# Kernel tuning notes

Hardware: AMD Instinct MI355X
Metric: run time of the kernel (lower is better)

## Reference

```python
import jax, jax.numpy as jnp
import numpy as np

NUM_ITEMS = 50000
IN_FEATS = 64
H_FEATS = 64
NUM_EDGES = 800000


def setup_inputs() -> dict:
    key = jax.random.key(0)
    ks = jax.random.split(key, 12)
    s_in = 1.0 / np.sqrt(IN_FEATS)
    s_h = 1.0 / np.sqrt(H_FEATS)
    return {
        "embed": jax.random.normal(ks[0], (NUM_ITEMS, IN_FEATS), jnp.float32),
        "W1_self": jax.random.normal(ks[1], (IN_FEATS, H_FEATS), jnp.float32) * s_in,
        "W1_neigh": jax.random.normal(ks[2], (IN_FEATS, H_FEATS), jnp.float32) * s_in,
        "b1": jax.random.normal(ks[3], (H_FEATS,), jnp.float32) * s_in,
        "W2_self": jax.random.normal(ks[4], (H_FEATS, H_FEATS), jnp.float32) * s_h,
        "W2_neigh": jax.random.normal(ks[5], (H_FEATS, H_FEATS), jnp.float32) * s_h,
        "b2": jax.random.normal(ks[6], (H_FEATS,), jnp.float32) * s_h,
        "W_fc": jax.random.normal(ks[7], (H_FEATS, IN_FEATS), jnp.float32) * s_h,
        "b_fc": jax.random.normal(ks[8], (IN_FEATS,), jnp.float32) * s_h,
        "item_ids": jnp.arange(NUM_ITEMS, dtype=jnp.int64),
        "src": jax.random.randint(ks[9], (NUM_EDGES,), 0, NUM_ITEMS, jnp.int64),
        "dst": jax.random.randint(ks[10], (NUM_EDGES,), 0, NUM_ITEMS, jnp.int64),
    }


def _sage_mean(h, src, dst, W_self, W_neigh, b, num_nodes):
    # gather src features along edges, mean-reduce into dst nodes
    agg = jax.ops.segment_sum(h[src], dst, num_segments=num_nodes)  # [N, d]
    deg = jax.ops.segment_sum(jnp.ones_like(dst, dtype=h.dtype), dst,
                              num_segments=num_nodes)
    h_neigh = agg / jnp.clip(deg, 1.0, None)[:, None]  # zero for isolated nodes
    return h @ W_self + h_neigh @ W_neigh + b


def reference(embed, W1_self, W1_neigh, b1, W2_self, W2_neigh, b2,
              W_fc, b_fc, item_ids, src, dst):
    n = embed.shape[0]
    x = embed[item_ids]                                   # embedding lookup [N, in]
    h = _sage_mean(x, src, dst, W1_self, W1_neigh, b1, n)  # SAGEConv 1
    h = jax.nn.relu(h)
    h = _sage_mean(h, src, dst, W2_self, W2_neigh, b2, n)  # SAGEConv 2
    return h @ W_fc + b_fc                                 # final linear
```

## Files before the change

kernel.cpp:

```cpp
#include <hip/hip_runtime.h>

#define NN 50000
#define NE 800000
#define F  64
#define AT 68
#define SCAN_B 49

__device__ __forceinline__ unsigned bf16rne(float f) {
    unsigned u = __float_as_uint(f);
    return (u + 0x7fffu + ((u >> 16) & 1u)) >> 16;
}
__device__ __forceinline__ float bflo(unsigned p) { return __uint_as_float(p << 16); }
__device__ __forceinline__ float bfhi(unsigned p) { return __uint_as_float(p & 0xffff0000u); }


__launch_bounds__(256)
__global__ void k_count_gather(const int* __restrict__ dst, int* __restrict__ cnt,
                               int* __restrict__ pos,
                               const float* __restrict__ embed, const int* __restrict__ ids,
                               uint2* __restrict__ xb) {
    int t = blockIdx.x * blockDim.x + threadIdx.x;
    if (t < NE) pos[t] = atomicAdd(&cnt[dst[t]], 1);
    if (t < NN * 16) {
        int i = t >> 4, c = t & 15;
        float4 v = ((const float4*)embed)[ids[i] * 16 + c];
        uint2 p;
        p.x = bf16rne(v.x) | (bf16rne(v.y) << 16);
        p.y = bf16rne(v.z) | (bf16rne(v.w) << 16);
        xb[t] = p;
    }
}


__launch_bounds__(256)
__global__ void k_scan_a(const int* __restrict__ cnt, int* __restrict__ partials) {
    __shared__ int sc[256];
    int t = threadIdx.x;
    int base = blockIdx.x * 1024 + t * 4;
    int s = 0;
#pragma unroll
    for (int k = 0; k < 4; ++k) {
        int idx = base + k;
        s += (idx < NN) ? cnt[idx] : 0;
    }
    sc[t] = s;
    __syncthreads();
    for (int d = 128; d > 0; d >>= 1) {
        if (t < d) sc[t] += sc[t + d];
        __syncthreads();
    }
    if (t == 0) partials[blockIdx.x] = sc[0];
}

__launch_bounds__(256)
__global__ void k_scan_c2(const int* __restrict__ cnt, const int* __restrict__ partials,
                          int* __restrict__ offs) {
    __shared__ int sboff;
    __shared__ int stotal;
    __shared__ int sc[256];
    int t = threadIdx.x;
    if (t < 64) {
        int v = (t < SCAN_B) ? partials[t] : 0;
        int orig = v;
        for (int d = 1; d < 64; d <<= 1) {
            int u = __shfl_up(v, d);
            if (t >= d) v += u;
        }
        if (t == (int)blockIdx.x) sboff = v - orig;
        if (t == 63) stotal = v;
    }
    int base = blockIdx.x * 1024 + t * 4;
    int v4[4];
#pragma unroll
    for (int k = 0; k < 4; ++k) {
        int idx = base + k;
        v4[k] = (idx < NN) ? cnt[idx] : 0;
    }
    int lsum = v4[0] + v4[1] + v4[2] + v4[3];
    sc[t] = lsum;
    __syncthreads();
    for (int d = 1; d < 256; d <<= 1) {
        int u = (t >= d) ? sc[t - d] : 0;
        __syncthreads();
        sc[t] += u;
        __syncthreads();
    }
    int run = sboff + sc[t] - lsum;
#pragma unroll
    for (int k = 0; k < 4; ++k) {
        int idx = base + k;
        if (idx < NN) { offs[idx] = run; run += v4[k]; }
    }
    if (blockIdx.x == 0 && t == 0) offs[NN] = stotal;
}

__global__ void k_fill(const int* __restrict__ src, const int* __restrict__ dst,
                       const int* __restrict__ offs, const int* __restrict__ pos,
                       int* __restrict__ csr) {
    int e = blockIdx.x * blockDim.x + threadIdx.x;
    if (e < NE) csr[offs[dst[e]] + pos[e]] = src[e];
}


__device__ __forceinline__ void add8(float s[8], const uint4 v) {
    s[0] += bflo(v.x); s[1] += bfhi(v.x);
    s[2] += bflo(v.y); s[3] += bfhi(v.y);
    s[4] += bflo(v.z); s[5] += bfhi(v.z);
    s[6] += bflo(v.w); s[7] += bfhi(v.w);
}

__launch_bounds__(256)
__global__ void k_aggb(const uint4* __restrict__ inb, const int* __restrict__ offs,
                       const int* __restrict__ csr, uint4* __restrict__ hnb) {
    int g = (blockIdx.x * 256 + threadIdx.x) >> 3;
    int c = threadIdx.x & 7;
    if (g >= NN) return;
    int lane = threadIdx.x & 63;
    int base = lane & 56;
    int beg = offs[g], end = offs[g + 1];
    float s[8] = {0.f, 0.f, 0.f, 0.f, 0.f, 0.f, 0.f, 0.f};
    int j = beg;
    for (; j + 8 <= end; j += 8) {
        int v = csr[j + c];
        int i0 = __shfl(v, base + 0, 64), i1 = __shfl(v, base + 1, 64);
        int i2 = __shfl(v, base + 2, 64), i3 = __shfl(v, base + 3, 64);
        int i4 = __shfl(v, base + 4, 64), i5 = __shfl(v, base + 5, 64);
        int i6 = __shfl(v, base + 6, 64), i7 = __shfl(v, base + 7, 64);
        uint4 d0 = inb[i0 * 8 + c], d1 = inb[i1 * 8 + c];
        uint4 d2 = inb[i2 * 8 + c], d3 = inb[i3 * 8 + c];
        uint4 d4 = inb[i4 * 8 + c], d5 = inb[i5 * 8 + c];
        uint4 d6 = inb[i6 * 8 + c], d7 = inb[i7 * 8 + c];
        add8(s, d0); add8(s, d1); add8(s, d2); add8(s, d3);
        add8(s, d4); add8(s, d5); add8(s, d6); add8(s, d7);
    }
    int rem = end - j;
    if (rem > 0) {
        int v = csr[j + (c < rem ? c : 0)];
        int idx[8];
#pragma unroll
        for (int k = 0; k < 8; ++k) idx[k] = __shfl(v, base + k, 64);
#pragma unroll
        for (int k = 0; k < 8; ++k)
            if (k < rem) { uint4 d = inb[idx[k] * 8 + c]; add8(s, d); }
    }
    int deg = end - beg;
    float inv = (deg > 0) ? 1.f / (float)deg : 0.f;
    uint4 o;
    o.x = bf16rne(s[0] * inv) | (bf16rne(s[1] * inv) << 16);
    o.y = bf16rne(s[2] * inv) | (bf16rne(s[3] * inv) << 16);
    o.z = bf16rne(s[4] * inv) | (bf16rne(s[5] * inv) << 16);
    o.w = bf16rne(s[6] * inv) | (bf16rne(s[7] * inv) << 16);
    hnb[g * 8 + c] = o;
}


__launch_bounds__(256)
__global__ void k_layer_mid(const float* __restrict__ X, const int* __restrict__ ids,
                            const uint4* __restrict__ Nhb,
                            const float* __restrict__ Ws, const float* __restrict__ Wn,
                            const float* __restrict__ b, uint2* __restrict__ outb) {
    __shared__ alignas(16) float AsT[F * AT];
    __shared__ alignas(16) float NsT[F * AT];
    __shared__ alignas(16) float WsL[F * F];
    __shared__ alignas(16) float WnL[F * F];

    const int tid = threadIdx.x;
    const int node0 = blockIdx.x * 64;

    for (int idx = tid; idx < F * F / 4; idx += 256) {
        ((float4*)WsL)[idx] = ((const float4*)Ws)[idx];
        ((float4*)WnL)[idx] = ((const float4*)Wn)[idx];
    }
    for (int idx = tid; idx < 64 * 16; idx += 256) {
        int n = idx >> 4, c = idx & 15;
        int node = node0 + n;
        float4 a = make_float4(0.f, 0.f, 0.f, 0.f);
        if (node < NN) a = ((const float4*)X)[ids[node] * 16 + c];
        int f = 4 * c;
        AsT[(f + 0) * AT + n] = a.x; AsT[(f + 1) * AT + n] = a.y;
        AsT[(f + 2) * AT + n] = a.z; AsT[(f + 3) * AT + n] = a.w;
    }
    for (int idx = tid; idx < 64 * 8; idx += 256) {
        int n = idx >> 3, c = idx & 7;
        int node = node0 + n;
        uint4 v = make_uint4(0u, 0u, 0u, 0u);
        if (node < NN) v = Nhb[node * 8 + c];
        int f = 8 * c;
        NsT[(f + 0) * AT + n] = bflo(v.x); NsT[(f + 1) * AT + n] = bfhi(v.x);
        NsT[(f + 2) * AT + n] = bflo(v.y); NsT[(f + 3) * AT + n] = bfhi(v.y);
        NsT[(f + 4) * AT + n] = bflo(v.z); NsT[(f + 5) * AT + n] = bfhi(v.z);
        NsT[(f + 6) * AT + n] = bflo(v.w); NsT[(f + 7) * AT + n] = bfhi(v.w);
    }
    __syncthreads();

    const int tx = tid & 15, ty = tid >> 4;
    float acc[4][4];
#pragma unroll
    for (int j = 0; j < 4; ++j) {
        float bv = b[4 * tx + j];
        acc[0][j] = bv; acc[1][j] = bv; acc[2][j] = bv; acc[3][j] = bv;
    }
#pragma unroll 4
    for (int k = 0; k < 64; ++k) {
        float4 a4 = *(const float4*)&AsT[k * AT + 4 * ty];
        float4 n4 = *(const float4*)&NsT[k * AT + 4 * ty];
        float4 w4 = *(const float4*)&WsL[k * 64 + 4 * tx];
        float4 u4 = *(const float4*)&WnL[k * 64 + 4 * tx];
        float a_[4] = {a4.x, a4.y, a4.z, a4.w};
        float n_[4] = {n4.x, n4.y, n4.z, n4.w};
        float w_[4] = {w4.x, w4.y, w4.z, w4.w};
        float u_[4] = {u4.x, u4.y, u4.z, u4.w};
#pragma unroll
        for (int i = 0; i < 4; ++i)
#pragma unroll
            for (int j = 0; j < 4; ++j)
                acc[i][j] += a_[i] * w_[j] + n_[i] * u_[j];
    }

#pragma unroll
    for (int i = 0; i < 4; ++i) {
        int node = node0 + 4 * ty + i;
        if (node < NN) {
            float ox = acc[i][0] > 0.f ? acc[i][0] : 0.f;
            float oy = acc[i][1] > 0.f ? acc[i][1] : 0.f;
            float oz = acc[i][2] > 0.f ? acc[i][2] : 0.f;
            float ow = acc[i][3] > 0.f ? acc[i][3] : 0.f;
            uint2 p;
            p.x = bf16rne(ox) | (bf16rne(oy) << 16);
            p.y = bf16rne(oz) | (bf16rne(ow) << 16);
            outb[node * 16 + tx] = p;
        }
    }
}


__launch_bounds__(256)
__global__ void k_layer_last(const uint4* __restrict__ Ab, const uint4* __restrict__ Nhb,
                             const float* __restrict__ Ws, const float* __restrict__ Wn,
                             const float* __restrict__ b,
                             const float* __restrict__ Wfc, const float* __restrict__ bfc,
                             float* __restrict__ out) {
    __shared__ alignas(16) float AsT[F * AT];
    __shared__ alignas(16) float NsT[F * AT];
    __shared__ alignas(16) float WsL[F * F];
    __shared__ alignas(16) float WnL[F * F];

    const int tid = threadIdx.x;
    const int node0 = blockIdx.x * 64;

    for (int idx = tid; idx < F * F / 4; idx += 256) {
        ((float4*)WsL)[idx] = ((const float4*)Ws)[idx];
        ((float4*)WnL)[idx] = ((const float4*)Wn)[idx];
    }
    for (int idx = tid; idx < 64 * 8; idx += 256) {
        int n = idx >> 3, c = idx & 7;
        int node = node0 + n;
        uint4 v = make_uint4(0u, 0u, 0u, 0u);
        if (node < NN) v = Ab[node * 8 + c];
        int f = 8 * c;
        AsT[(f + 0) * AT + n] = bflo(v.x); AsT[(f + 1) * AT + n] = bfhi(v.x);
        AsT[(f + 2) * AT + n] = bflo(v.y); AsT[(f + 3) * AT + n] = bfhi(v.y);
        AsT[(f + 4) * AT + n] = bflo(v.z); AsT[(f + 5) * AT + n] = bfhi(v.z);
        AsT[(f + 6) * AT + n] = bflo(v.w); AsT[(f + 7) * AT + n] = bfhi(v.w);
    }
    for (int idx = tid; idx < 64 * 8; idx += 256) {
        int n = idx >> 3, c = idx & 7;
        int node = node0 + n;
        uint4 v = make_uint4(0u, 0u, 0u, 0u);
        if (node < NN) v = Nhb[node * 8 + c];
        int f = 8 * c;
        NsT[(f + 0) * AT + n] = bflo(v.x); NsT[(f + 1) * AT + n] = bfhi(v.x);
        NsT[(f + 2) * AT + n] = bflo(v.y); NsT[(f + 3) * AT + n] = bfhi(v.y);
        NsT[(f + 4) * AT + n] = bflo(v.z); NsT[(f + 5) * AT + n] = bfhi(v.z);
        NsT[(f + 6) * AT + n] = bflo(v.w); NsT[(f + 7) * AT + n] = bfhi(v.w);
    }
    __syncthreads();

    const int tx = tid & 15, ty = tid >> 4;
    float acc[4][4];
#pragma unroll
    for (int j = 0; j < 4; ++j) {
        float bv = b[4 * tx + j];
        acc[0][j] = bv; acc[1][j] = bv; acc[2][j] = bv; acc[3][j] = bv;
    }
#pragma unroll 4
    for (int k = 0; k < 64; ++k) {
        float4 a4 = *(const float4*)&AsT[k * AT + 4 * ty];
        float4 n4 = *(const float4*)&NsT[k * AT + 4 * ty];
        float4 w4 = *(const float4*)&WsL[k * 64 + 4 * tx];
        float4 u4 = *(const float4*)&WnL[k * 64 + 4 * tx];
        float a_[4] = {a4.x, a4.y, a4.z, a4.w};
        float n_[4] = {n4.x, n4.y, n4.z, n4.w};
        float w_[4] = {w4.x, w4.y, w4.z, w4.w};
        float u_[4] = {u4.x, u4.y, u4.z, u4.w};
#pragma unroll
        for (int i = 0; i < 4; ++i)
#pragma unroll
            for (int j = 0; j < 4; ++j)
                acc[i][j] += a_[i] * w_[j] + n_[i] * u_[j];
    }

    __syncthreads();
#pragma unroll
    for (int i = 0; i < 4; ++i)
#pragma unroll
        for (int j = 0; j < 4; ++j)
            AsT[(4 * tx + j) * AT + (4 * ty + i)] = acc[i][j];
    for (int idx = tid; idx < F * F / 4; idx += 256)
        ((float4*)WsL)[idx] = ((const float4*)Wfc)[idx];
    __syncthreads();

    float acc2[4][4];
#pragma unroll
    for (int j = 0; j < 4; ++j) {
        float bv = bfc[4 * tx + j];
        acc2[0][j] = bv; acc2[1][j] = bv; acc2[2][j] = bv; acc2[3][j] = bv;
    }
#pragma unroll 4
    for (int k = 0; k < 64; ++k) {
        float4 a4 = *(const float4*)&AsT[k * AT + 4 * ty];
        float4 w4 = *(const float4*)&WsL[k * 64 + 4 * tx];
        float a_[4] = {a4.x, a4.y, a4.z, a4.w};
        float w_[4] = {w4.x, w4.y, w4.z, w4.w};
#pragma unroll
        for (int i = 0; i < 4; ++i)
#pragma unroll
            for (int j = 0; j < 4; ++j)
                acc2[i][j] += a_[i] * w_[j];
    }
#pragma unroll
    for (int i = 0; i < 4; ++i) {
        int node = node0 + 4 * ty + i;
        if (node < NN) {
            float4 o;
            o.x = acc2[i][0]; o.y = acc2[i][1]; o.z = acc2[i][2]; o.w = acc2[i][3];
            *(float4*)&out[node * 64 + 4 * tx] = o;
        }
    }
}


extern "C" void kernel_launch(void* const* d_in, const int* in_sizes, int n_in,
                              void* d_out, int out_size, void* d_ws, size_t ws_size,
                              hipStream_t stream) {
    const float* embed = (const float*)d_in[0];
    const float* W1s = (const float*)d_in[1];
    const float* W1n = (const float*)d_in[2];
    const float* b1  = (const float*)d_in[3];
    const float* W2s = (const float*)d_in[4];
    const float* W2n = (const float*)d_in[5];
    const float* b2  = (const float*)d_in[6];
    const float* Wfc = (const float*)d_in[7];
    const float* bfc = (const float*)d_in[8];
    const int* ids = (const int*)d_in[9];
    const int* src = (const int*)d_in[10];
    const int* dst = (const int*)d_in[11];
    float* out = (float*)d_out;

    char* ws = (char*)d_ws;
    size_t off = 0;
    auto alloc = [&](size_t nb) {
        char* p = ws + off;
        off = (off + nb + 255) & ~(size_t)255;
        return p;
    };
    int*   cnt      = (int*)alloc(NN * sizeof(int));
    size_t zero_bytes = off;
    int*   offs     = (int*)alloc((NN + 1) * sizeof(int));
    int*   partials = (int*)alloc(SCAN_B * sizeof(int));
    int*   pos      = (int*)alloc(NE * sizeof(int));
    int*   csr      = (int*)alloc(NE * sizeof(int));
    uint2* xb       = (uint2*)alloc((size_t)NN * 16 * sizeof(uint2));
    uint2* h1b      = (uint2*)alloc((size_t)NN * 16 * sizeof(uint2));
    uint4* hnb      = (uint4*)alloc((size_t)NN * 8 * sizeof(uint4));

    hipMemsetAsync(d_ws, 0, zero_bytes, stream);

    const int TB = 256;
    const int EB = (NE + TB - 1) / TB;
    k_count_gather<<<EB, TB, 0, stream>>>(dst, cnt, pos, embed, ids, xb);
    k_scan_a<<<SCAN_B, 256, 0, stream>>>(cnt, partials);
    k_scan_c2<<<SCAN_B, 256, 0, stream>>>(cnt, partials, offs);
    k_fill<<<EB, TB, 0, stream>>>(src, dst, offs, pos, csr);

    const int NB = (NN + 63) / 64;
    const int AB = (NN * 8 + 255) / 256;

    k_aggb<<<AB, TB, 0, stream>>>((const uint4*)xb, offs, csr, hnb);
    k_layer_mid<<<NB, TB, 0, stream>>>(embed, ids, hnb, W1s, W1n, b1, h1b);
    k_aggb<<<AB, TB, 0, stream>>>((const uint4*)h1b, offs, csr, hnb);
    k_layer_last<<<NB, TB, 0, stream>>>((const uint4*)h1b, hnb, W2s, W2n, b2, Wfc, bfc, out);
}
```

Measured before the change: 236.0 us.

## Sort aggregation nodes by degree and unroll gather by sixteen edges

Builds a degree histogram during the scan and a new kernel that writes a permutation grouping nodes by in-degree. The aggregation kernel then visits nodes in that order, so the 8-lane groups in a wavefront have similar edge counts, and its gather loop now handles 16 edges per iteration. Layer 1 reads the bf16 copy of the embeddings instead of gathering fp32 rows, so the self term now uses bf16-rounded input. This adds a kernel launch and extra atomics, and scatters the output writes.

```diff
diff --git a/kernel.cpp b/kernel.cpp
--- a/kernel.cpp
+++ b/kernel.cpp
@@ -54,10 +54,11 @@
 
 __launch_bounds__(256)
 __global__ void k_scan_c2(const int* __restrict__ cnt, const int* __restrict__ partials,
-                          int* __restrict__ offs) {
+                          int* __restrict__ offs, int* __restrict__ dhist) {
     __shared__ int sboff;
     __shared__ int stotal;
     __shared__ int sc[256];
+    __shared__ int shist[64];
     int t = threadIdx.x;
     if (t < 64) {
         int v = (t < SCAN_B) ? partials[t] : 0;
@@ -68,6 +69,7 @@
         }
         if (t == (int)blockIdx.x) sboff = v - orig;
         if (t == 63) stotal = v;
+        shist[t] = 0;
     }
     int base = blockIdx.x * 1024 + t * 4;
     int v4[4];
@@ -79,6 +81,11 @@
     int lsum = v4[0] + v4[1] + v4[2] + v4[3];
     sc[t] = lsum;
     __syncthreads();
+#pragma unroll
+    for (int k = 0; k < 4; ++k) {
+        int idx = base + k;
+        if (idx < NN) atomicAdd(&shist[v4[k] < 63 ? v4[k] : 63], 1);
+    }
     for (int d = 1; d < 256; d <<= 1) {
         int u = (t >= d) ? sc[t - d] : 0;
         __syncthreads();
@@ -92,6 +99,44 @@
         if (idx < NN) { offs[idx] = run; run += v4[k]; }
     }
     if (blockIdx.x == 0 && t == 0) offs[NN] = stotal;
+    if (t < 64 && shist[t]) atomicAdd(&dhist[t], shist[t]);
+}
+
+
+__launch_bounds__(256)
+__global__ void k_perm(const int* __restrict__ cnt, const int* __restrict__ dhist,
+                       int* __restrict__ dcur, int* __restrict__ perm) {
+    __shared__ int boff[64];
+    __shared__ int bcnt[64];
+    __shared__ int bbase[64];
+    __shared__ int bcur[64];
+    int t = threadIdx.x;
+    int node = blockIdx.x * 256 + t;
+    if (t < 64) {
+        int v = dhist[t];
+        int orig = v;
+        for (int d = 1; d < 64; d <<= 1) {
+            int u = __shfl_up(v, d);
+            if (t >= d) v += u;
+        }
+        boff[t] = v - orig;
+        bcnt[t] = 0;
+        bcur[t] = 0;
+    }
+    __syncthreads();
+    int bin = -1;
+    if (node < NN) {
+        int deg = cnt[node];
+        bin = deg < 63 ? deg : 63;
+        atomicAdd(&bcnt[bin], 1);
+    }
+    __syncthreads();
+    if (t < 64) bbase[t] = bcnt[t] ? atomicAdd(&dcur[t], bcnt[t]) : 0;
+    __syncthreads();
+    if (node < NN) {
+        int p = atomicAdd(&bcur[bin], 1);
+        perm[boff[bin] + bbase[bin] + p] = node;
+    }
 }
 
 __global__ void k_fill(const int* __restrict__ src, const int* __restrict__ dst,
@@ -111,15 +156,41 @@
 
 __launch_bounds__(256)
 __global__ void k_aggb(const uint4* __restrict__ inb, const int* __restrict__ offs,
-                       const int* __restrict__ csr, uint4* __restrict__ hnb) {
-    int g = (blockIdx.x * 256 + threadIdx.x) >> 3;
+                       const int* __restrict__ csr, const int* __restrict__ perm,
+                       uint4* __restrict__ hnb) {
+    int gg = (blockIdx.x * 256 + threadIdx.x) >> 3;
     int c = threadIdx.x & 7;
-    if (g >= NN) return;
+    if (gg >= NN) return;
+    int node = perm[gg];
     int lane = threadIdx.x & 63;
     int base = lane & 56;
-    int beg = offs[g], end = offs[g + 1];
+    int beg = offs[node], end = offs[node + 1];
     float s[8] = {0.f, 0.f, 0.f, 0.f, 0.f, 0.f, 0.f, 0.f};
     int j = beg;
+    for (; j + 16 <= end; j += 16) {
+        int va = csr[j + c];
+        int vb = csr[j + 8 + c];
+        int i0 = __shfl(va, base + 0, 64), i1 = __shfl(va, base + 1, 64);
+        int i2 = __shfl(va, base + 2, 64), i3 = __shfl(va, base + 3, 64);
+        int i4 = __shfl(va, base + 4, 64), i5 = __shfl(va, base + 5, 64);
+        int i6 = __shfl(va, base + 6, 64), i7 = __shfl(va, base + 7, 64);
+        int m0 = __shfl(vb, base + 0, 64), m1 = __shfl(vb, base + 1, 64);
+        int m2 = __shfl(vb, base + 2, 64), m3 = __shfl(vb, base + 3, 64);
+        int m4 = __shfl(vb, base + 4, 64), m5 = __shfl(vb, base + 5, 64);
+        int m6 = __shfl(vb, base + 6, 64), m7 = __shfl(vb, base + 7, 64);
+        uint4 d0 = inb[i0 * 8 + c], d1 = inb[i1 * 8 + c];
+        uint4 d2 = inb[i2 * 8 + c], d3 = inb[i3 * 8 + c];
+        uint4 d4 = inb[i4 * 8 + c], d5 = inb[i5 * 8 + c];
+        uint4 d6 = inb[i6 * 8 + c], d7 = inb[i7 * 8 + c];
+        uint4 e0 = inb[m0 * 8 + c], e1 = inb[m1 * 8 + c];
+        uint4 e2 = inb[m2 * 8 + c], e3 = inb[m3 * 8 + c];
+        uint4 e4 = inb[m4 * 8 + c], e5 = inb[m5 * 8 + c];
+        uint4 e6 = inb[m6 * 8 + c], e7 = inb[m7 * 8 + c];
+        add8(s, d0); add8(s, d1); add8(s, d2); add8(s, d3);
+        add8(s, d4); add8(s, d5); add8(s, d6); add8(s, d7);
+        add8(s, e0); add8(s, e1); add8(s, e2); add8(s, e3);
+        add8(s, e4); add8(s, e5); add8(s, e6); add8(s, e7);
+    }
     for (; j + 8 <= end; j += 8) {
         int v = csr[j + c];
         int i0 = __shfl(v, base + 0, 64), i1 = __shfl(v, base + 1, 64);
@@ -150,15 +221,17 @@
     o.y = bf16rne(s[2] * inv) | (bf16rne(s[3] * inv) << 16);
     o.z = bf16rne(s[4] * inv) | (bf16rne(s[5] * inv) << 16);
     o.w = bf16rne(s[6] * inv) | (bf16rne(s[7] * inv) << 16);
-    hnb[g * 8 + c] = o;
-}
-
-
-__launch_bounds__(256)
-__global__ void k_layer_mid(const float* __restrict__ X, const int* __restrict__ ids,
-                            const uint4* __restrict__ Nhb,
-                            const float* __restrict__ Ws, const float* __restrict__ Wn,
-                            const float* __restrict__ b, uint2* __restrict__ outb) {
+    hnb[node * 8 + c] = o;
+}
+
+
+template <bool LAST>
+__launch_bounds__(256)
+__global__ void k_layer(const uint4* __restrict__ Ab, const uint4* __restrict__ Nhb,
+                        const float* __restrict__ Ws, const float* __restrict__ Wn,
+                        const float* __restrict__ b,
+                        const float* __restrict__ Wfc, const float* __restrict__ bfc,
+                        uint2* __restrict__ outb, float* __restrict__ out) {
     __shared__ alignas(16) float AsT[F * AT];
     __shared__ alignas(16) float NsT[F * AT];
     __shared__ alignas(16) float WsL[F * F];
@@ -171,21 +244,20 @@
         ((float4*)WsL)[idx] = ((const float4*)Ws)[idx];
         ((float4*)WnL)[idx] = ((const float4*)Wn)[idx];
     }
-    for (int idx = tid; idx < 64 * 16; idx += 256) {
-        int n = idx >> 4, c = idx & 15;
-        int node = node0 + n;
-        float4 a = make_float4(0.f, 0.f, 0.f, 0.f);
-        if (node < NN) a = ((const float4*)X)[ids[node] * 16 + c];
-        int f = 4 * c;
-        AsT[(f + 0) * AT + n] = a.x; AsT[(f + 1) * AT + n] = a.y;
-        AsT[(f + 2) * AT + n] = a.z; AsT[(f + 3) * AT + n] = a.w;
-    }
     for (int idx = tid; idx < 64 * 8; idx += 256) {
         int n = idx >> 3, c = idx & 7;
         int node = node0 + n;
+        uint4 a = make_uint4(0u, 0u, 0u, 0u);
         uint4 v = make_uint4(0u, 0u, 0u, 0u);
-        if (node < NN) v = Nhb[node * 8 + c];
+        if (node < NN) {
+            a = Ab[node * 8 + c];
+            v = Nhb[node * 8 + c];
+        }
         int f = 8 * c;
+        AsT[(f + 0) * AT + n] = bflo(a.x); AsT[(f + 1) * AT + n] = bfhi(a.x);
+        AsT[(f + 2) * AT + n] = bflo(a.y); AsT[(f + 3) * AT + n] = bfhi(a.y);
+        AsT[(f + 4) * AT + n] = bflo(a.z); AsT[(f + 5) * AT + n] = bfhi(a.z);
+        AsT[(f + 6) * AT + n] = bflo(a.w); AsT[(f + 7) * AT + n] = bfhi(a.w);
         NsT[(f + 0) * AT + n] = bflo(v.x); NsT[(f + 1) * AT + n] = bfhi(v.x);
         NsT[(f + 2) * AT + n] = bflo(v.y); NsT[(f + 3) * AT + n] = bfhi(v.y);
         NsT[(f + 4) * AT + n] = bflo(v.z); NsT[(f + 5) * AT + n] = bfhi(v.z);
@@ -217,124 +289,58 @@
                 acc[i][j] += a_[i] * w_[j] + n_[i] * u_[j];
     }
 
-#pragma unroll
-    for (int i = 0; i < 4; ++i) {
-        int node = node0 + 4 * ty + i;
-        if (node < NN) {
-            float ox = acc[i][0] > 0.f ? acc[i][0] : 0.f;
-            float oy = acc[i][1] > 0.f ? acc[i][1] : 0.f;
-            float oz = acc[i][2] > 0.f ? acc[i][2] : 0.f;
-            float ow = acc[i][3] > 0.f ? acc[i][3] : 0.f;
-            uint2 p;
-            p.x = bf16rne(ox) | (bf16rne(oy) << 16);
-            p.y = bf16rne(oz) | (bf16rne(ow) << 16);
-            outb[node * 16 + tx] = p;
-        }
-    }
-}
-
-
-__launch_bounds__(256)
-__global__ void k_layer_last(const uint4* __restrict__ Ab, const uint4* __restrict__ Nhb,
-                             const float* __restrict__ Ws, const float* __restrict__ Wn,
-                             const float* __restrict__ b,
-                             const float* __restrict__ Wfc, const float* __restrict__ bfc,
-                             float* __restrict__ out) {
-    __shared__ alignas(16) float AsT[F * AT];
-    __shared__ alignas(16) float NsT[F * AT];
-    __shared__ alignas(16) float WsL[F * F];
-    __shared__ alignas(16) float WnL[F * F];
-
-    const int tid = threadIdx.x;
-    const int node0 = blockIdx.x * 64;
-
-    for (int idx = tid; idx < F * F / 4; idx += 256) {
-        ((float4*)WsL)[idx] = ((const float4*)Ws)[idx];
-        ((float4*)WnL)[idx] = ((const float4*)Wn)[idx];
-    }
-    for (int idx = tid; idx < 64 * 8; idx += 256) {
-        int n = idx >> 3, c = idx & 7;
-        int node = node0 + n;
-        uint4 v = make_uint4(0u, 0u, 0u, 0u);
-        if (node < NN) v = Ab[node * 8 + c];
-        int f = 8 * c;
-        AsT[(f + 0) * AT + n] = bflo(v.x); AsT[(f + 1) * AT + n] = bfhi(v.x);
-        AsT[(f + 2) * AT + n] = bflo(v.y); AsT[(f + 3) * AT + n] = bfhi(v.y);
-        AsT[(f + 4) * AT + n] = bflo(v.z); AsT[(f + 5) * AT + n] = bfhi(v.z);
-        AsT[(f + 6) * AT + n] = bflo(v.w); AsT[(f + 7) * AT + n] = bfhi(v.w);
-    }
-    for (int idx = tid; idx < 64 * 8; idx += 256) {
-        int n = idx >> 3, c = idx & 7;
-        int node = node0 + n;
-        uint4 v = make_uint4(0u, 0u, 0u, 0u);
-        if (node < NN) v = Nhb[node * 8 + c];
-        int f = 8 * c;
-        NsT[(f + 0) * AT + n] = bflo(v.x); NsT[(f + 1) * AT + n] = bfhi(v.x);
-        NsT[(f + 2) * AT + n] = bflo(v.y); NsT[(f + 3) * AT + n] = bfhi(v.y);
-        NsT[(f + 4) * AT + n] = bflo(v.z); NsT[(f + 5) * AT + n] = bfhi(v.z);
-        NsT[(f + 6) * AT + n] = bflo(v.w); NsT[(f + 7) * AT + n] = bfhi(v.w);
-    }
-    __syncthreads();
-
-    const int tx = tid & 15, ty = tid >> 4;
-    float acc[4][4];
-#pragma unroll
-    for (int j = 0; j < 4; ++j) {
-        float bv = b[4 * tx + j];
-        acc[0][j] = bv; acc[1][j] = bv; acc[2][j] = bv; acc[3][j] = bv;
-    }
+    if (!LAST) {
+#pragma unroll
+        for (int i = 0; i < 4; ++i) {
+            int node = node0 + 4 * ty + i;
+            if (node < NN) {
+                float ox = acc[i][0] > 0.f ? acc[i][0] : 0.f;
+                float oy = acc[i][1] > 0.f ? acc[i][1] : 0.f;
+                float oz = acc[i][2] > 0.f ? acc[i][2] : 0.f;
+                float ow = acc[i][3] > 0.f ? acc[i][3] : 0.f;
+                uint2 p;
+                p.x = bf16rne(ox) | (bf16rne(oy) << 16);
+                p.y = bf16rne(oz) | (bf16rne(ow) << 16);
+                outb[node * 16 + tx] = p;
+            }
+        }
+    } else {
+        __syncthreads();
+#pragma unroll
+        for (int i = 0; i < 4; ++i)
+#pragma unroll
+            for (int j = 0; j < 4; ++j)
+                AsT[(4 * tx + j) * AT + (4 * ty + i)] = acc[i][j];
+        for (int idx = tid; idx < F * F / 4; idx += 256)
+            ((float4*)WsL)[idx] = ((const float4*)Wfc)[idx];
+        __syncthreads();
+
+        float acc2[4][4];
+#pragma unroll
+        for (int j = 0; j < 4; ++j) {
+            float bv = bfc[4 * tx + j];
+            acc2[0][j] = bv; acc2[1][j] = bv; acc2[2][j] = bv; acc2[3][j] = bv;
+        }
 #pragma unroll 4
-    for (int k = 0; k < 64; ++k) {
-        float4 a4 = *(const float4*)&AsT[k * AT + 4 * ty];
-        float4 n4 = *(const float4*)&NsT[k * AT + 4 * ty];
-        float4 w4 = *(const float4*)&WsL[k * 64 + 4 * tx];
-        float4 u4 = *(const float4*)&WnL[k * 64 + 4 * tx];
-        float a_[4] = {a4.x, a4.y, a4.z, a4.w};
-        float n_[4] = {n4.x, n4.y, n4.z, n4.w};
-        float w_[4] = {w4.x, w4.y, w4.z, w4.w};
-        float u_[4] = {u4.x, u4.y, u4.z, u4.w};
-#pragma unroll
-        for (int i = 0; i < 4; ++i)
-#pragma unroll
-            for (int j = 0; j < 4; ++j)
-                acc[i][j] += a_[i] * w_[j] + n_[i] * u_[j];
-    }
-
-    __syncthreads();
-#pragma unroll
-    for (int i = 0; i < 4; ++i)
-#pragma unroll
-        for (int j = 0; j < 4; ++j)
-            AsT[(4 * tx + j) * AT + (4 * ty + i)] = acc[i][j];
-    for (int idx = tid; idx < F * F / 4; idx += 256)
-        ((float4*)WsL)[idx] = ((const float4*)Wfc)[idx];
-    __syncthreads();
-
-    float acc2[4][4];
-#pragma unroll
-    for (int j = 0; j < 4; ++j) {
-        float bv = bfc[4 * tx + j];
-        acc2[0][j] = bv; acc2[1][j] = bv; acc2[2][j] = bv; acc2[3][j] = bv;
-    }
-#pragma unroll 4
-    for (int k = 0; k < 64; ++k) {
-        float4 a4 = *(const float4*)&AsT[k * AT + 4 * ty];
-        float4 w4 = *(const float4*)&WsL[k * 64 + 4 * tx];
-        float a_[4] = {a4.x, a4.y, a4.z, a4.w};
-        float w_[4] = {w4.x, w4.y, w4.z, w4.w};
-#pragma unroll
-        for (int i = 0; i < 4; ++i)
-#pragma unroll
-            for (int j = 0; j < 4; ++j)
-                acc2[i][j] += a_[i] * w_[j];
-    }
-#pragma unroll
-    for (int i = 0; i < 4; ++i) {
-        int node = node0 + 4 * ty + i;
-        if (node < NN) {
-            float4 o;
-            o.x = acc2[i][0]; o.y = acc2[i][1]; o.z = acc2[i][2]; o.w = acc2[i][3];
-            *(float4*)&out[node * 64 + 4 * tx] = o;
+        for (int k = 0; k < 64; ++k) {
+            float4 a4 = *(const float4*)&AsT[k * AT + 4 * ty];
+            float4 w4 = *(const float4*)&WsL[k * 64 + 4 * tx];
+            float a_[4] = {a4.x, a4.y, a4.z, a4.w};
+            float w_[4] = {w4.x, w4.y, w4.z, w4.w};
+#pragma unroll
+            for (int i = 0; i < 4; ++i)
+#pragma unroll
+                for (int j = 0; j < 4; ++j)
+                    acc2[i][j] += a_[i] * w_[j];
+        }
+#pragma unroll
+        for (int i = 0; i < 4; ++i) {
+            int node = node0 + 4 * ty + i;
+            if (node < NN) {
+                float4 o;
+                o.x = acc2[i][0]; o.y = acc2[i][1]; o.z = acc2[i][2]; o.w = acc2[i][3];
+                *(float4*)&out[node * 64 + 4 * tx] = o;
+            }
         }
     }
 }
@@ -365,9 +371,12 @@
         return p;
     };
     int*   cnt      = (int*)alloc(NN * sizeof(int));
+    int*   dhist    = (int*)alloc(64 * sizeof(int));
+    int*   dcur     = (int*)alloc(64 * sizeof(int));
     size_t zero_bytes = off;
     int*   offs     = (int*)alloc((NN + 1) * sizeof(int));
     int*   partials = (int*)alloc(SCAN_B * sizeof(int));
+    int*   perm     = (int*)alloc(NN * sizeof(int));
     int*   pos      = (int*)alloc(NE * sizeof(int));
     int*   csr      = (int*)alloc(NE * sizeof(int));
     uint2* xb       = (uint2*)alloc((size_t)NN * 16 * sizeof(uint2));
@@ -380,14 +389,17 @@
     const int EB = (NE + TB - 1) / TB;
     k_count_gather<<<EB, TB, 0, stream>>>(dst, cnt, pos, embed, ids, xb);
     k_scan_a<<<SCAN_B, 256, 0, stream>>>(cnt, partials);
-    k_scan_c2<<<SCAN_B, 256, 0, stream>>>(cnt, partials, offs);
+    k_scan_c2<<<SCAN_B, 256, 0, stream>>>(cnt, partials, offs, dhist);
+    k_perm<<<(NN + 255) / 256, 256, 0, stream>>>(cnt, dhist, dcur, perm);
     k_fill<<<EB, TB, 0, stream>>>(src, dst, offs, pos, csr);
 
     const int NB = (NN + 63) / 64;
     const int AB = (NN * 8 + 255) / 256;
 
-    k_aggb<<<AB, TB, 0, stream>>>((const uint4*)xb, offs, csr, hnb);
-    k_layer_mid<<<NB, TB, 0, stream>>>(embed, ids, hnb, W1s, W1n, b1, h1b);
-    k_aggb<<<AB, TB, 0, stream>>>((const uint4*)h1b, offs, csr, hnb);
-    k_layer_last<<<NB, TB, 0, stream>>>((const uint4*)h1b, hnb, W2s, W2n, b2, Wfc, bfc, out);
-}
+    k_aggb<<<AB, TB, 0, stream>>>((const uint4*)xb, offs, csr, perm, hnb);
+    k_layer<false><<<NB, TB, 0, stream>>>((const uint4*)xb, hnb, W1s, W1n, b1,
+                                          nullptr, nullptr, h1b, nullptr);
+    k_aggb<<<AB, TB, 0, stream>>>((const uint4*)h1b, offs, csr, perm, hnb);
+    k_layer<true><<<NB, TB, 0, stream>>>((const uint4*)h1b, hnb, W2s, W2n, b2,
+                                         Wfc, bfc, nullptr, out);
+}
```

Result: no change. 235.3 us (-0.3%).

## Fuse neighbor aggregation into SAGE layer GEMM kernels with 512-thread blocks

Applied to the files above, without the earlier changes.

Merges the CSR mean-aggregation kernel into each layer's GEMM kernel, so neighbor sums go straight into shared memory instead of through a bf16 intermediate buffer in global memory. This removes two launches and the write and re-read of that buffer. Blocks grow to 512 threads with 2 rows per thread. Weights are packed as bf16 pairs in LDS, which cuts shared memory use but lowers weight precision. Layer 1 now reads the bf16 embedding copy rather than fp32 embed, and the mean is kept in fp32 instead of being rounded to bf16.

```diff
diff --git a/kernel.cpp b/kernel.cpp
--- a/kernel.cpp
+++ b/kernel.cpp
@@ -109,232 +109,149 @@
     s[6] += bflo(v.w); s[7] += bfhi(v.w);
 }
 
-__launch_bounds__(256)
-__global__ void k_aggb(const uint4* __restrict__ inb, const int* __restrict__ offs,
-                       const int* __restrict__ csr, uint4* __restrict__ hnb) {
-    int g = (blockIdx.x * 256 + threadIdx.x) >> 3;
-    int c = threadIdx.x & 7;
-    if (g >= NN) return;
-    int lane = threadIdx.x & 63;
-    int base = lane & 56;
-    int beg = offs[g], end = offs[g + 1];
-    float s[8] = {0.f, 0.f, 0.f, 0.f, 0.f, 0.f, 0.f, 0.f};
-    int j = beg;
-    for (; j + 8 <= end; j += 8) {
-        int v = csr[j + c];
-        int i0 = __shfl(v, base + 0, 64), i1 = __shfl(v, base + 1, 64);
-        int i2 = __shfl(v, base + 2, 64), i3 = __shfl(v, base + 3, 64);
-        int i4 = __shfl(v, base + 4, 64), i5 = __shfl(v, base + 5, 64);
-        int i6 = __shfl(v, base + 6, 64), i7 = __shfl(v, base + 7, 64);
-        uint4 d0 = inb[i0 * 8 + c], d1 = inb[i1 * 8 + c];
-        uint4 d2 = inb[i2 * 8 + c], d3 = inb[i3 * 8 + c];
-        uint4 d4 = inb[i4 * 8 + c], d5 = inb[i5 * 8 + c];
-        uint4 d6 = inb[i6 * 8 + c], d7 = inb[i7 * 8 + c];
-        add8(s, d0); add8(s, d1); add8(s, d2); add8(s, d3);
-        add8(s, d4); add8(s, d5); add8(s, d6); add8(s, d7);
-    }
-    int rem = end - j;
-    if (rem > 0) {
-        int v = csr[j + (c < rem ? c : 0)];
-        int idx[8];
-#pragma unroll
-        for (int k = 0; k < 8; ++k) idx[k] = __shfl(v, base + k, 64);
-#pragma unroll
-        for (int k = 0; k < 8; ++k)
-            if (k < rem) { uint4 d = inb[idx[k] * 8 + c]; add8(s, d); }
-    }
-    int deg = end - beg;
-    float inv = (deg > 0) ? 1.f / (float)deg : 0.f;
-    uint4 o;
-    o.x = bf16rne(s[0] * inv) | (bf16rne(s[1] * inv) << 16);
-    o.y = bf16rne(s[2] * inv) | (bf16rne(s[3] * inv) << 16);
-    o.z = bf16rne(s[4] * inv) | (bf16rne(s[5] * inv) << 16);
-    o.w = bf16rne(s[6] * inv) | (bf16rne(s[7] * inv) << 16);
-    hnb[g * 8 + c] = o;
-}
-
-
-__launch_bounds__(256)
-__global__ void k_layer_mid(const float* __restrict__ X, const int* __restrict__ ids,
-                            const uint4* __restrict__ Nhb,
-                            const float* __restrict__ Ws, const float* __restrict__ Wn,
-                            const float* __restrict__ b, uint2* __restrict__ outb) {
+template <bool LAST>
+__launch_bounds__(512)
+__global__ void k_fused(const uint4* __restrict__ Ab, const int* __restrict__ offs,
+                        const int* __restrict__ csr,
+                        const float* __restrict__ Ws, const float* __restrict__ Wn,
+                        const float* __restrict__ b,
+                        const float* __restrict__ Wfc, const float* __restrict__ bfc,
+                        uint2* __restrict__ outb, float* __restrict__ out) {
     __shared__ alignas(16) float AsT[F * AT];
     __shared__ alignas(16) float NsT[F * AT];
-    __shared__ alignas(16) float WsL[F * F];
-    __shared__ alignas(16) float WnL[F * F];
+    __shared__ alignas(16) unsigned Wpk[F * F];
 
     const int tid = threadIdx.x;
     const int node0 = blockIdx.x * 64;
 
-    for (int idx = tid; idx < F * F / 4; idx += 256) {
-        ((float4*)WsL)[idx] = ((const float4*)Ws)[idx];
-        ((float4*)WnL)[idx] = ((const float4*)Wn)[idx];
-    }
-    for (int idx = tid; idx < 64 * 16; idx += 256) {
-        int n = idx >> 4, c = idx & 15;
-        int node = node0 + n;
-        float4 a = make_float4(0.f, 0.f, 0.f, 0.f);
-        if (node < NN) a = ((const float4*)X)[ids[node] * 16 + c];
-        int f = 4 * c;
-        AsT[(f + 0) * AT + n] = a.x; AsT[(f + 1) * AT + n] = a.y;
-        AsT[(f + 2) * AT + n] = a.z; AsT[(f + 3) * AT + n] = a.w;
-    }
-    for (int idx = tid; idx < 64 * 8; idx += 256) {
-        int n = idx >> 3, c = idx & 7;
-        int node = node0 + n;
-        uint4 v = make_uint4(0u, 0u, 0u, 0u);
-        if (node < NN) v = Nhb[node * 8 + c];
+    for (int i = tid; i < F * F; i += 512)
+        Wpk[i] = bf16rne(Ws[i]) | (bf16rne(Wn[i]) << 16);
+
+    {
+        const int n = tid >> 3;
+        const int c = tid & 7;
+        const int lane = tid & 63;
+        const int base = lane & 56;
+        const int gnode = node0 + n;
+        float s[8] = {0.f, 0.f, 0.f, 0.f, 0.f, 0.f, 0.f, 0.f};
+        uint4 a = make_uint4(0u, 0u, 0u, 0u);
+        float inv = 0.f;
+        if (gnode < NN) {
+            a = Ab[gnode * 8 + c];
+            int beg = offs[gnode], end = offs[gnode + 1];
+            int j = beg;
+            for (; j + 8 <= end; j += 8) {
+                int v = csr[j + c];
+                int i0 = __shfl(v, base + 0, 64), i1 = __shfl(v, base + 1, 64);
+                int i2 = __shfl(v, base + 2, 64), i3 = __shfl(v, base + 3, 64);
+                int i4 = __shfl(v, base + 4, 64), i5 = __shfl(v, base + 5, 64);
+                int i6 = __shfl(v, base + 6, 64), i7 = __shfl(v, base + 7, 64);
+                uint4 d0 = Ab[i0 * 8 + c], d1 = Ab[i1 * 8 + c];
+                uint4 d2 = Ab[i2 * 8 + c], d3 = Ab[i3 * 8 + c];
+                uint4 d4 = Ab[i4 * 8 + c], d5 = Ab[i5 * 8 + c];
+                uint4 d6 = Ab[i6 * 8 + c], d7 = Ab[i7 * 8 + c];
+                add8(s, d0); add8(s, d1); add8(s, d2); add8(s, d3);
+                add8(s, d4); add8(s, d5); add8(s, d6); add8(s, d7);
+            }
+            int rem = end - j;
+            if (rem > 0) {
+                int v = csr[j + (c < rem ? c : 0)];
+                int idx[8];
+#pragma unroll
+                for (int k = 0; k < 8; ++k) idx[k] = __shfl(v, base + k, 64);
+#pragma unroll
+                for (int k = 0; k < 8; ++k)
+                    if (k < rem) { uint4 d = Ab[idx[k] * 8 + c]; add8(s, d); }
+            }
+            int deg = end - beg;
+            inv = (deg > 0) ? 1.f / (float)deg : 0.f;
+        }
         int f = 8 * c;
-        NsT[(f + 0) * AT + n] = bflo(v.x); NsT[(f + 1) * AT + n] = bfhi(v.x);
-        NsT[(f + 2) * AT + n] = bflo(v.y); NsT[(f + 3) * AT + n] = bfhi(v.y);
-        NsT[(f + 4) * AT + n] = bflo(v.z); NsT[(f + 5) * AT + n] = bfhi(v.z);
-        NsT[(f + 6) * AT + n] = bflo(v.w); NsT[(f + 7) * AT + n] = bfhi(v.w);
+        AsT[(f + 0) * AT + n] = bflo(a.x); AsT[(f + 1) * AT + n] = bfhi(a.x);
+        AsT[(f + 2) * AT + n] = bflo(a.y); AsT[(f + 3) * AT + n] = bfhi(a.y);
+        AsT[(f + 4) * AT + n] = bflo(a.z); AsT[(f + 5) * AT + n] = bfhi(a.z);
+        AsT[(f + 6) * AT + n] = bflo(a.w); AsT[(f + 7) * AT + n] = bfhi(a.w);
+#pragma unroll
+        for (int q = 0; q < 8; ++q) NsT[(f + q) * AT + n] = s[q] * inv;
     }
     __syncthreads();
 
     const int tx = tid & 15, ty = tid >> 4;
-    float acc[4][4];
+    float acc[2][4];
 #pragma unroll
     for (int j = 0; j < 4; ++j) {
         float bv = b[4 * tx + j];
-        acc[0][j] = bv; acc[1][j] = bv; acc[2][j] = bv; acc[3][j] = bv;
+        acc[0][j] = bv; acc[1][j] = bv;
     }
 #pragma unroll 4
     for (int k = 0; k < 64; ++k) {
-        float4 a4 = *(const float4*)&AsT[k * AT + 4 * ty];
-        float4 n4 = *(const float4*)&NsT[k * AT + 4 * ty];
-        float4 w4 = *(const float4*)&WsL[k * 64 + 4 * tx];
-        float4 u4 = *(const float4*)&WnL[k * 64 + 4 * tx];
-        float a_[4] = {a4.x, a4.y, a4.z, a4.w};
-        float n_[4] = {n4.x, n4.y, n4.z, n4.w};
-        float w_[4] = {w4.x, w4.y, w4.z, w4.w};
-        float u_[4] = {u4.x, u4.y, u4.z, u4.w};
-#pragma unroll
-        for (int i = 0; i < 4; ++i)
+        float2 a2 = *(const float2*)&AsT[k * AT + 2 * ty];
+        float2 n2 = *(const float2*)&NsT[k * AT + 2 * ty];
+        uint4 wq = *(const uint4*)&Wpk[k * 64 + 4 * tx];
+        float ws_[4] = {bflo(wq.x), bflo(wq.y), bflo(wq.z), bflo(wq.w)};
+        float wn_[4] = {bfhi(wq.x), bfhi(wq.y), bfhi(wq.z), bfhi(wq.w)};
+        float a_[2] = {a2.x, a2.y};
+        float n_[2] = {n2.x, n2.y};
+#pragma unroll
+        for (int i = 0; i < 2; ++i)
 #pragma unroll
             for (int j = 0; j < 4; ++j)
-                acc[i][j] += a_[i] * w_[j] + n_[i] * u_[j];
-    }
-
-#pragma unroll
-    for (int i = 0; i < 4; ++i) {
-        int node = node0 + 4 * ty + i;
-        if (node < NN) {
-            float ox = acc[i][0] > 0.f ? acc[i][0] : 0.f;
-            float oy = acc[i][1] > 0.f ? acc[i][1] : 0.f;
-            float oz = acc[i][2] > 0.f ? acc[i][2] : 0.f;
-            float ow = acc[i][3] > 0.f ? acc[i][3] : 0.f;
-            uint2 p;
-            p.x = bf16rne(ox) | (bf16rne(oy) << 16);
-            p.y = bf16rne(oz) | (bf16rne(ow) << 16);
-            outb[node * 16 + tx] = p;
-        }
-    }
-}
-
-
-__launch_bounds__(256)
-__global__ void k_layer_last(const uint4* __restrict__ Ab, const uint4* __restrict__ Nhb,
-                             const float* __restrict__ Ws, const float* __restrict__ Wn,
-                             const float* __restrict__ b,
-                             const float* __restrict__ Wfc, const float* __restrict__ bfc,
-                             float* __restrict__ out) {
-    __shared__ alignas(16) float AsT[F * AT];
-    __shared__ alignas(16) float NsT[F * AT];
-    __shared__ alignas(16) float WsL[F * F];
-    __shared__ alignas(16) float WnL[F * F];
-
-    const int tid = threadIdx.x;
-    const int node0 = blockIdx.x * 64;
-
-    for (int idx = tid; idx < F * F / 4; idx += 256) {
-        ((float4*)WsL)[idx] = ((const float4*)Ws)[idx];
-        ((float4*)WnL)[idx] = ((const float4*)Wn)[idx];
-    }
-    for (int idx = tid; idx < 64 * 8; idx += 256) {
-        int n = idx >> 3, c = idx & 7;
-        int node = node0 + n;
-        uint4 v = make_uint4(0u, 0u, 0u, 0u);
-        if (node < NN) v = Ab[node * 8 + c];
-        int f = 8 * c;
-        AsT[(f + 0) * AT + n] = bflo(v.x); AsT[(f + 1) * AT + n] = bfhi(v.x);
-        AsT[(f + 2) * AT + n] = bflo(v.y); AsT[(f + 3) * AT + n] = bfhi(v.y);
-        AsT[(f + 4) * AT + n] = bflo(v.z); AsT[(f + 5) * AT + n] = bfhi(v.z);
-        AsT[(f + 6) * AT + n] = bflo(v.w); AsT[(f + 7) * AT + n] = bfhi(v.w);
-    }
-    for (int idx = tid; idx < 64 * 8; idx += 256) {
-        int n = idx >> 3, c = idx & 7;
-        int node = node0 + n;
-        uint4 v = make_uint4(0u, 0u, 0u, 0u);
-        if (node < NN) v = Nhb[node * 8 + c];
-        int f = 8 * c;
-        NsT[(f + 0) * AT + n] = bflo(v.x); NsT[(f + 1) * AT + n] = bfhi(v.x);
-        NsT[(f + 2) * AT + n] = bflo(v.y); NsT[(f + 3) * AT + n] = bfhi(v.y);
-        NsT[(f + 4) * AT + n] = bflo(v.z); NsT[(f + 5) * AT + n] = bfhi(v.z);
-        NsT[(f + 6) * AT + n] = bflo(v.w); NsT[(f + 7) * AT + n] = bfhi(v.w);
-    }
-    __syncthreads();
-
-    const int tx = tid & 15, ty = tid >> 4;
-    float acc[4][4];
-#pragma unroll
-    for (int j = 0; j < 4; ++j) {
-        float bv = b[4 * tx + j];
-        acc[0][j] = bv; acc[1][j] = bv; acc[2][j] = bv; acc[3][j] = bv;
-    }
+                acc[i][j] += a_[i] * ws_[j] + n_[i] * wn_[j];
+    }
+
+    if (!LAST) {
+#pragma unroll
+        for (int i = 0; i < 2; ++i) {
+            int node = node0 + 2 * ty + i;
+            if (node < NN) {
+                float o0 = acc[i][0] > 0.f ? acc[i][0] : 0.f;
+                float o1 = acc[i][1] > 0.f ? acc[i][1] : 0.f;
+                float o2 = acc[i][2] > 0.f ? acc[i][2] : 0.f;
+                float o3 = acc[i][3] > 0.f ? acc[i][3] : 0.f;
+                uint2 p;
+                p.x = bf16rne(o0) | (bf16rne(o1) << 16);
+                p.y = bf16rne(o2) | (bf16rne(o3) << 16);
+                outb[node * 16 + tx] = p;
+            }
+        }
+    } else {
+        __syncthreads();
+        float* Wf = (float*)Wpk;
+#pragma unroll
+        for (int i = 0; i < 2; ++i)
+#pragma unroll
+            for (int j = 0; j < 4; ++j)
+                AsT[(4 * tx + j) * AT + (2 * ty + i)] = acc[i][j];
+        for (int i = tid; i < F * F / 4; i += 512)
+            ((float4*)Wf)[i] = ((const float4*)Wfc)[i];
+        __syncthreads();
+
+        float acc2[2][4];
+#pragma unroll
+        for (int j = 0; j < 4; ++j) {
+            float bv = bfc[4 * tx + j];
+            acc2[0][j] = bv; acc2[1][j] = bv;
+        }
 #pragma unroll 4
-    for (int k = 0; k < 64; ++k) {
-        float4 a4 = *(const float4*)&AsT[k * AT + 4 * ty];
-        float4 n4 = *(const float4*)&NsT[k * AT + 4 * ty];
-        float4 w4 = *(const float4*)&WsL[k * 64 + 4 * tx];
-        float4 u4 = *(const float4*)&WnL[k * 64 + 4 * tx];
-        float a_[4] = {a4.x, a4.y, a4.z, a4.w};
-        float n_[4] = {n4.x, n4.y, n4.z, n4.w};
-        float w_[4] = {w4.x, w4.y, w4.z, w4.w};
-        float u_[4] = {u4.x, u4.y, u4.z, u4.w};
-#pragma unroll
-        for (int i = 0; i < 4; ++i)
-#pragma unroll
-            for (int j = 0; j < 4; ++j)
-                acc[i][j] += a_[i] * w_[j] + n_[i] * u_[j];
-    }
-
-    __syncthreads();
-#pragma unroll
-    for (int i = 0; i < 4; ++i)
-#pragma unroll
-        for (int j = 0; j < 4; ++j)
-            AsT[(4 * tx + j) * AT + (4 * ty + i)] = acc[i][j];
-    for (int idx = tid; idx < F * F / 4; idx += 256)
-        ((float4*)WsL)[idx] = ((const float4*)Wfc)[idx];
-    __syncthreads();
-
-    float acc2[4][4];
-#pragma unroll
-    for (int j = 0; j < 4; ++j) {
-        float bv = bfc[4 * tx + j];
-        acc2[0][j] = bv; acc2[1][j] = bv; acc2[2][j] = bv; acc2[3][j] = bv;
-    }
-#pragma unroll 4
-    for (int k = 0; k < 64; ++k) {
-        float4 a4 = *(const float4*)&AsT[k * AT + 4 * ty];
-        float4 w4 = *(const float4*)&WsL[k * 64 + 4 * tx];
-        float a_[4] = {a4.x, a4.y, a4.z, a4.w};
-        float w_[4] = {w4.x, w4.y, w4.z, w4.w};
-#pragma unroll
-        for (int i = 0; i < 4; ++i)
-#pragma unroll
-            for (int j = 0; j < 4; ++j)
-                acc2[i][j] += a_[i] * w_[j];
-    }
-#pragma unroll
-    for (int i = 0; i < 4; ++i) {
-        int node = node0 + 4 * ty + i;
-        if (node < NN) {
-            float4 o;
-            o.x = acc2[i][0]; o.y = acc2[i][1]; o.z = acc2[i][2]; o.w = acc2[i][3];
-            *(float4*)&out[node * 64 + 4 * tx] = o;
+        for (int k = 0; k < 64; ++k) {
+            float2 a2 = *(const float2*)&AsT[k * AT + 2 * ty];
+            float4 w4 = *(const float4*)&Wf[k * 64 + 4 * tx];
+            float a_[2] = {a2.x, a2.y};
+            float w_[4] = {w4.x, w4.y, w4.z, w4.w};
+#pragma unroll
+            for (int i = 0; i < 2; ++i)
+#pragma unroll
+                for (int j = 0; j < 4; ++j)
+                    acc2[i][j] += a_[i] * w_[j];
+        }
+#pragma unroll
+        for (int i = 0; i < 2; ++i) {
+            int node = node0 + 2 * ty + i;
+            if (node < NN) {
+                float4 o;
+                o.x = acc2[i][0]; o.y = acc2[i][1]; o.z = acc2[i][2]; o.w = acc2[i][3];
+                *(float4*)&out[node * 64 + 4 * tx] = o;
+            }
         }
     }
 }
@@ -372,7 +289,6 @@
     int*   csr      = (int*)alloc(NE * sizeof(int));
     uint2* xb       = (uint2*)alloc((size_t)NN * 16 * sizeof(uint2));
     uint2* h1b      = (uint2*)alloc((size_t)NN * 16 * sizeof(uint2));
-    uint4* hnb      = (uint4*)alloc((size_t)NN * 8 * sizeof(uint4));
 
     hipMemsetAsync(d_ws, 0, zero_bytes, stream);
 
@@ -384,10 +300,10 @@
     k_fill<<<EB, TB, 0, stream>>>(src, dst, offs, pos, csr);
 
     const int NB = (NN + 63) / 64;
-    const int AB = (NN * 8 + 255) / 256;
-
-    k_aggb<<<AB, TB, 0, stream>>>((const uint4*)xb, offs, csr, hnb);
-    k_layer_mid<<<NB, TB, 0, stream>>>(embed, ids, hnb, W1s, W1n, b1, h1b);
-    k_aggb<<<AB, TB, 0, stream>>>((const uint4*)h1b, offs, csr, hnb);
-    k_layer_last<<<NB, TB, 0, stream>>>((const uint4*)h1b, hnb, W2s, W2n, b2, Wfc, bfc, out);
-}
+    k_fused<false><<<NB, 512, 0, stream>>>((const uint4*)xb, offs, csr,
+                                           W1s, W1n, b1, nullptr, nullptr,
+                                           h1b, nullptr);
+    k_fused<true><<<NB, 512, 0, stream>>>((const uint4*)h1b, offs, csr,
+                                          W2s, W2n, b2, Wfc, bfc,
+                                          nullptr, out);
+}
```

New measurement: 231.6 us (median of 2 runs). About the same (-1.9%).
